# Kernel optimization log

Hardware: AMD Instinct MI355X
Metric: run time of the kernel (lower is better)

The kernel has to match this reference:

```python
import jax, jax.numpy as jnp
import numpy as np

B, T, C = 1, 2048, 2048
N_HEAD, N_KV = 32, 8
HD = C // N_HEAD            # 64
N_REP = N_HEAD // N_KV      # 4
WINDOW = 512                # sliding_window
N_GLOBAL = 16               # n_global_tokens


def setup_inputs() -> dict:
    key = jax.random.key(0)
    ks = jax.random.split(key, 5)
    x = jax.random.normal(ks[0], (B, T, C), jnp.float32)
    # standard RoPE frequency tables, shape (T, HD//2)
    inv_freq = 1.0 / (10000.0 ** (np.arange(0, HD, 2, dtype=np.float32) / HD))
    ang = np.outer(np.arange(T, dtype=np.float32), inv_freq)
    freqs_cos = jnp.asarray(np.cos(ang), jnp.float32)
    freqs_sin = jnp.asarray(np.sin(ang), jnp.float32)
    s = 0.02
    wq = jax.random.normal(ks[1], (C, C), jnp.float32) * s
    wk = jax.random.normal(ks[2], (N_KV * HD, C), jnp.float32) * s
    wv = jax.random.normal(ks[3], (N_KV * HD, C), jnp.float32) * s
    wo = jax.random.normal(ks[4], (C, C), jnp.float32) * s
    return {"x": x, "freqs_cos": freqs_cos, "freqs_sin": freqs_sin,
            "wq": wq, "wk": wk, "wv": wv, "wo": wo}


def _apply_rope(xh, fc, fs):
    # xh: (B, H, T, HD); fc/fs: (T, HD//2) broadcast over (B, H)
    xr = xh.reshape(*xh.shape[:-1], HD // 2, 2)
    x0, x1 = xr[..., 0], xr[..., 1]
    fc = fc[None, None]
    fs = fs[None, None]
    out = jnp.stack([x0 * fc - x1 * fs, x0 * fs + x1 * fc], axis=-1)
    return out.reshape(xh.shape)


def reference(x, freqs_cos, freqs_sin, wq, wk, wv, wo):
    Bx, Tx, Cx = x.shape
    q = (x @ wq.T).reshape(Bx, Tx, N_HEAD, HD).transpose(0, 2, 1, 3)   # (B,Hq,T,hd)
    k = (x @ wk.T).reshape(Bx, Tx, N_KV, HD).transpose(0, 2, 1, 3)     # (B,Hkv,T,hd)
    v = (x @ wv.T).reshape(Bx, Tx, N_KV, HD).transpose(0, 2, 1, 3)
    q = _apply_rope(q, freqs_cos, freqs_sin)
    k = _apply_rope(k, freqs_cos, freqs_sin)

    # GQA: group query heads over shared kv heads instead of repeat_kv
    qg = q.reshape(Bx, N_KV, N_REP, Tx, HD)
    scale = 1.0 / float(np.sqrt(HD))
    scores = jnp.einsum('bgrqd,bgkd->bgrqk', qg, k) * scale  # (B,G,R,T,T)

    # sliding-window causal mask with global tokens (kv_cache=None branch)
    q_pos = jnp.arange(Tx)[:, None]
    k_pos = jnp.arange(Tx)[None, :]
    mask = (k_pos <= q_pos) & (k_pos >= q_pos - (WINDOW - 1))
    mask = mask | (k_pos < N_GLOBAL)
    # note: global columns combined with causal rows always leave >=1 valid key
    scores = jnp.where(mask[None, None, None], scores, -jnp.inf)
    probs = jax.nn.softmax(scores, axis=-1)

    y = jnp.einsum('bgrqk,bgkd->bgrqd', probs, v)
    y = y.reshape(Bx, N_HEAD, Tx, HD).transpose(0, 2, 1, 3).reshape(Bx, Tx, Cx)
    return y @ wo.T  # dropout p=0 in eval
```

## Files before the change

### kernel.cpp

```cpp
#include <hip/hip_runtime.h>
#include <hip/hip_bf16.h>

using short8 = __attribute__((ext_vector_type(8))) short;
using f32x4  = __attribute__((ext_vector_type(4))) float;
using f32x16 = __attribute__((ext_vector_type(16))) float;
using int4v  = __attribute__((ext_vector_type(4))) int;

#define T_SEQ  2048
#define C_DIM  2048
#define NH     32
#define NKV    8
#define HD     64
#define WINDOW 512
#define NGLOB  16

__device__ inline ushort f2bf(float f) {
  union { float f; unsigned u; } v; v.f = f;
  unsigned u = v.u;
  u += 0x7fffu + ((u >> 16) & 1u);
  return (ushort)(u >> 16);
}
__device__ inline float bf2f(ushort h) {
  union { unsigned u; float f; } v; v.u = ((unsigned)h) << 16;
  return v.f;
}

__device__ __forceinline__ void gl_lds16(const ushort* g, ushort* l) {
  __builtin_amdgcn_global_load_lds(
      (const __attribute__((address_space(1))) void*)g,
      (__attribute__((address_space(3))) void*)l, 16, 0, 0);
}

__device__ __forceinline__ f32x16 zero16() {
  f32x16 v;
#pragma unroll
  for (int i = 0; i < 16; i++) v[i] = 0.f;
  return v;
}

__global__ void cvt_all(const float* __restrict__ s0, ushort* __restrict__ d0, int n0,
                        const float* __restrict__ s1, ushort* __restrict__ d1, int n1,
                        const float* __restrict__ s2, ushort* __restrict__ d2, int n2,
                        const float* __restrict__ s3, ushort* __restrict__ d3, int n3,
                        const float* __restrict__ s4, ushort* __restrict__ d4, int n4) {
  int total = n0 + n1 + n2 + n3 + n4;
  int stride = gridDim.x * blockDim.x;
  for (int i = blockIdx.x * blockDim.x + threadIdx.x; i < total; i += stride) {
    int j = i; const float* s; ushort* d;
    if (j < n0) { s = s0; d = d0; }
    else { j -= n0;
      if (j < n1) { s = s1; d = d1; }
      else { j -= n1;
        if (j < n2) { s = s2; d = d2; }
        else { j -= n2;
          if (j < n3) { s = s3; d = d3; }
          else { j -= n3; s = s4; d = d4; } } } }
    f32x4 a = *reinterpret_cast<const f32x4*>(s + (size_t)j * 8);
    f32x4 b = *reinterpret_cast<const f32x4*>(s + (size_t)j * 8 + 4);
    short8 o;
#pragma unroll
    for (int k = 0; k < 4; k++) { o[k] = (short)f2bf(a[k]); o[4 + k] = (short)f2bf(b[k]); }
    *reinterpret_cast<short8*>(d + (size_t)j * 8) = o;
  }
}

template <int MODE>
__global__ __launch_bounds__(512) void gemm2p(const ushort* __restrict__ A,
                                              const ushort* __restrict__ B0,
                                              const ushort* __restrict__ B1,
                                              const ushort* __restrict__ B2,
                                              void* __restrict__ C0,
                                              void* __restrict__ C1,
                                              void* __restrict__ C2,
                                              int K) {
  __shared__ ushort As[2][2][128][32];
  __shared__ ushort Bs[2][2][128][32];
  const int tid  = threadIdx.x;
  const int lane = tid & 63;
  const int wid  = tid >> 6;
  const int wr = wid >> 2, wc = wid & 3;
  const int r16 = lane & 15, g16 = (lane >> 4) & 3;
  const int bx = blockIdx.x, by = blockIdx.y;

  const ushort* Brow;
  void* Cout;
  int ldc, col0;
  if constexpr (MODE == 1) {
    if (bx < 16)      { Brow = B0 + (size_t)bx * 128 * K;        Cout = C0; ldc = 2048; col0 = bx * 128; }
    else if (bx < 20) { Brow = B1 + (size_t)(bx - 16) * 128 * K; Cout = C1; ldc = 512;  col0 = (bx - 16) * 128; }
    else              { Brow = B2 + (size_t)(bx - 20) * 128 * K; Cout = C2; ldc = 512;  col0 = (bx - 20) * 128; }
  } else {
    Brow = B0 + (size_t)bx * 128 * K; Cout = C0; ldc = 2048; col0 = bx * 128;
  }
  const ushort* Arow = A + (size_t)by * 128 * K;

  f32x4 acc[4][2];
#pragma unroll
  for (int i = 0; i < 4; i++)
#pragma unroll
    for (int j = 0; j < 2; j++) acc[i][j] = (f32x4){0.f, 0.f, 0.f, 0.f};

  const int srow = tid >> 2, scch = tid & 3;
  const int ssc  = scch ^ ((srow >> 1) & 3);
  const size_t agoff = (size_t)srow * K + ssc * 8;
  const int rchunk = (g16 ^ ((r16 >> 1) & 3)) * 8;

  const int nt = K >> 6;
  int d = 0;

#define STAGE(dd, k0)                                                         \
  {                                                                           \
    _Pragma("unroll") for (int kk = 0; kk < 2; kk++) {                        \
      gl_lds16(&Arow[agoff + (k0) + kk * 32], &As[dd][kk][srow][scch * 8]);   \
      gl_lds16(&Brow[agoff + (k0) + kk * 32], &Bs[dd][kk][srow][scch * 8]);   \
    }                                                                         \
  }

  STAGE(0, 0);
  __syncthreads();

  for (int t = 0; t < nt; ++t) {
    if (t + 1 < nt) STAGE(d ^ 1, (t + 1) * 64);
#pragma unroll
    for (int kk = 0; kk < 2; kk++) {
      short8 af[4], bfv[2];
#pragma unroll
      for (int i = 0; i < 4; i++)
        af[i] = *reinterpret_cast<const short8*>(&As[d][kk][wr * 64 + i * 16 + r16][rchunk]);
#pragma unroll
      for (int j = 0; j < 2; j++)
        bfv[j] = *reinterpret_cast<const short8*>(&Bs[d][kk][wc * 32 + j * 16 + r16][rchunk]);
#pragma unroll
      for (int i = 0; i < 4; i++)
#pragma unroll
        for (int j = 0; j < 2; j++)
          acc[i][j] = __builtin_amdgcn_mfma_f32_16x16x32_bf16(af[i], bfv[j], acc[i][j], 0, 0, 0);
    }
    __syncthreads();
    d ^= 1;
  }
#undef STAGE

#pragma unroll
  for (int i = 0; i < 4; i++)
#pragma unroll
    for (int j = 0; j < 2; j++) {
      int col = col0 + wc * 32 + j * 16 + r16;
#pragma unroll
      for (int r = 0; r < 4; r++) {
        int row = by * 128 + wr * 64 + i * 16 + g16 * 4 + r;
        if constexpr (MODE == 0) ((float*)Cout)[(size_t)row * ldc + col] = acc[i][j][r];
        else                     ((ushort*)Cout)[(size_t)row * ldc + col] = f2bf(acc[i][j][r]);
      }
    }
}

__global__ void rope2(ushort* __restrict__ Qb, ushort* __restrict__ Kb,
                      const float* __restrict__ fc, const float* __restrict__ fs) {
  int idx = blockIdx.x * blockDim.x + threadIdx.x;
  const int QN = T_SEQ * NH * 8;
  ushort* X; int t, hh, c, ld; float ksc;
  if (idx < QN) { X = Qb; c = idx & 7; hh = (idx >> 3) & 31; t = idx >> 8; ld = NH * HD;
                  ksc = 0.125f * 1.44269504089f; }
  else { idx -= QN; X = Kb; c = idx & 7; hh = (idx >> 3) & 7; t = idx >> 6; ld = NKV * HD;
         ksc = 1.0f; }
  size_t base = (size_t)t * ld + hh * HD + c * 8;
  short8 v = *reinterpret_cast<const short8*>(&X[base]);
  f32x4 cc = *reinterpret_cast<const f32x4*>(&fc[t * 32 + c * 4]);
  f32x4 ss = *reinterpret_cast<const f32x4*>(&fs[t * 32 + c * 4]);
  short8 o;
#pragma unroll
  for (int j = 0; j < 4; j++) {
    float x0 = bf2f((ushort)v[2 * j]), x1 = bf2f((ushort)v[2 * j + 1]);
    o[2 * j]     = (short)f2bf((x0 * cc[j] - x1 * ss[j]) * ksc);
    o[2 * j + 1] = (short)f2bf((x0 * ss[j] + x1 * cc[j]) * ksc);
  }
  *reinterpret_cast<short8*>(&X[base]) = o;
}

__global__ __launch_bounds__(256) void transpose_bf16(const ushort* __restrict__ in,
                                                      ushort* __restrict__ out,
                                                      int R, int Cc) {
  __shared__ ushort tile[64][72];
  int tr = blockIdx.y * 64, tc = blockIdx.x * 64;
  int tid = threadIdx.x;
#pragma unroll
  for (int s = 0; s < 2; s++) {
    int idx = tid + s * 256;
    int row = idx >> 3, c8 = idx & 7;
    short8 v = *reinterpret_cast<const short8*>(&in[(size_t)(tr + row) * Cc + tc + c8 * 8]);
#pragma unroll
    for (int j = 0; j < 8; j++) tile[row][c8 * 8 + j] = (ushort)v[j];
  }
  __syncthreads();
#pragma unroll
  for (int s = 0; s < 2; s++) {
    int idx = tid + s * 256;
    int orow = idx >> 3, c8 = idx & 7;
    short8 v;
#pragma unroll
    for (int j = 0; j < 8; j++) v[j] = (short)tile[c8 * 8 + j][orow];
    *reinterpret_cast<short8*>(&out[(size_t)(tc + orow) * R + tr + c8 * 8]) = v;
  }
}

__global__ __launch_bounds__(256) void attn32(const ushort* __restrict__ Q,
                                              const ushort* __restrict__ K,
                                              const ushort* __restrict__ Vt,
                                              ushort* __restrict__ Y) {
  __shared__ ushort Ot[4][32][72];
  const int lane = threadIdx.x & 63;
  const int wv   = threadIdx.x >> 6;
  const int g  = blockIdx.x >> 6;
  const int qt = blockIdx.x & 63;
  const int h  = g * 4 + wv;
  const int q0 = qt << 5;
  const int l31 = lane & 31, hi = lane >> 5;
  const int hi8 = hi << 3, hi4 = hi << 2;
  const int qrow = q0 + l31;

  short8 qf[4];
#pragma unroll
  for (int s = 0; s < 4; s++)
    qf[s] = *reinterpret_cast<const short8*>(&Q[(size_t)qrow * C_DIM + h * HD + s * 16 + hi8]);

  f32x16 o[2] = { zero16(), zero16() };
  float mrow = -1e30f, ssum = 0.f;

  auto pack8 = [&](const float* pp) -> short8 {
    unsigned wA, wB, wC, wD;
    asm("v_cvt_pk_bf16_f32 %0, %1, %2" : "=v"(wA) : "v"(pp[0]), "v"(pp[1]));
    asm("v_cvt_pk_bf16_f32 %0, %1, %2" : "=v"(wB) : "v"(pp[2]), "v"(pp[3]));
    asm("v_cvt_pk_bf16_f32 %0, %1, %2" : "=v"(wC) : "v"(pp[4]), "v"(pp[5]));
    asm("v_cvt_pk_bf16_f32 %0, %1, %2" : "=v"(wD) : "v"(pp[6]), "v"(pp[7]));
    asm("v_permlane32_swap_b32 %0, %1" : "+v"(wA), "+v"(wC));
    asm("v_permlane32_swap_b32 %0, %1" : "+v"(wB), "+v"(wD));
    int4v w4 = { (int)wA, (int)wB, (int)wC, (int)wD };
    return __builtin_bit_cast(short8, w4);
  };

#define LOADKV(kreg, vreg, kb)                                                     \
  {                                                                                \
    _Pragma("unroll") for (int s = 0; s < 4; s++)                                  \
      kreg[s] = *reinterpret_cast<const short8*>(                                  \
          &K[(size_t)((kb) + l31) * (NKV * HD) + g * HD + s * 16 + hi8]);          \
    _Pragma("unroll") for (int ntl = 0; ntl < 2; ntl++) {                          \
      const ushort* vp = &Vt[(size_t)(g * HD + ntl * 32 + l31) * T_SEQ + (kb) + hi8]; \
      vreg[2 * ntl]     = *reinterpret_cast<const short8*>(vp);                    \
      vreg[2 * ntl + 1] = *reinterpret_cast<const short8*>(vp + 16);               \
    }                                                                              \
  }

#define PROCESS(kreg, vreg, kb, domask)                                            \
  {                                                                                \
    f32x16 sa = zero16();                                                          \
    __builtin_amdgcn_s_setprio(1);                                                 \
    _Pragma("unroll") for (int s = 0; s < 4; s++)                                  \
      sa = __builtin_amdgcn_mfma_f32_32x32x16_bf16(kreg[s], qf[s], sa, 0, 0, 0);   \
    __builtin_amdgcn_s_setprio(0);                                                 \
    float p[16];                                                                   \
    _Pragma("unroll") for (int r = 0; r < 16; r++) p[r] = sa[r];                   \
    if (domask) {                                                                  \
      _Pragma("unroll") for (int r = 0; r < 16; r++) {                             \
        int kidx = (kb) + (r & 3) + 8 * (r >> 2) + hi4;                            \
        bool ok = ((kidx <= qrow) && (kidx >= qrow - (WINDOW - 1))) || (kidx < NGLOB); \
        p[r] = ok ? p[r] : -1e30f;                                                 \
      }                                                                            \
    }                                                                              \
    float t[16];                                                                   \
    _Pragma("unroll") for (int r = 0; r < 16; r++) t[r] = p[r];                    \
    _Pragma("unroll") for (int st = 1; st < 16; st <<= 1)                          \
      _Pragma("unroll") for (int i2 = 0; i2 < 16; i2 += 2 * st)                    \
        t[i2] = fmaxf(t[i2], t[i2 + st]);                                          \
    float pmax = fmaxf(t[0], __shfl_xor(t[0], 32));                                \
    if (!__all(pmax <= mrow + 8.0f)) {                                             \
      float mnew = fmaxf(mrow, pmax);                                              \
      float corr = exp2f(mrow - mnew);                                             \
      ssum *= corr;                                                                \
      _Pragma("unroll") for (int r = 0; r < 16; r++) { o[0][r] *= corr; o[1][r] *= corr; } \
      mrow = mnew;                                                                 \
    }                                                                              \
    _Pragma("unroll") for (int r = 0; r < 16; r++) p[r] = exp2f(p[r] - mrow);      \
    float su[16];                                                                  \
    _Pragma("unroll") for (int r = 0; r < 16; r++) su[r] = p[r];                   \
    _Pragma("unroll") for (int st = 1; st < 16; st <<= 1)                          \
      _Pragma("unroll") for (int i2 = 0; i2 < 16; i2 += 2 * st)                    \
        su[i2] += su[i2 + st];                                                     \
    ssum += su[0];                                                                 \
    short8 pb0 = pack8(&p[0]);                                                     \
    short8 pb1 = pack8(&p[8]);                                                     \
    __builtin_amdgcn_s_setprio(1);                                                 \
    o[0] = __builtin_amdgcn_mfma_f32_32x32x16_bf16(vreg[0], pb0, o[0], 0, 0, 0);   \
    o[0] = __builtin_amdgcn_mfma_f32_32x32x16_bf16(vreg[1], pb1, o[0], 0, 0, 0);   \
    o[1] = __builtin_amdgcn_mfma_f32_32x32x16_bf16(vreg[2], pb0, o[1], 0, 0, 0);   \
    o[1] = __builtin_amdgcn_mfma_f32_32x32x16_bf16(vreg[3], pb1, o[1], 0, 0, 0);   \
    __builtin_amdgcn_s_setprio(0);                                                 \
  }

  int wsr = (q0 - (WINDOW - 1)) >> 5;
  int wstart = (wsr < 1) ? 32 : (wsr << 5);
  int ntw = (q0 >= wstart) ? (((q0 - wstart) >> 5) + 1) : 0;
  const int NT = 1 + ntw;

  short8 kA[4], vA[4], kB[4], vB[4];
  LOADKV(kA, vA, 0);

  for (int i = 0; i < NT; i += 2) {
    int kb_i = (i == 0) ? 0 : wstart + (i - 1) * 32;
    if (i + 1 < NT) { int kb1 = wstart + i * 32; LOADKV(kB, vB, kb1); }
    bool m_i = (i == 0) || (kb_i < q0 - 480) || (kb_i == q0);
    PROCESS(kA, vA, kb_i, m_i);
    if (i + 1 < NT) {
      int kb1 = wstart + i * 32;
      if (i + 2 < NT) { int kb2 = wstart + (i + 1) * 32; LOADKV(kA, vA, kb2); }
      bool m1 = (kb1 < q0 - 480) || (kb1 == q0);
      PROCESS(kB, vB, kb1, m1);
    }
  }
#undef LOADKV
#undef PROCESS

  float stot = ssum + __shfl_xor(ssum, 32);
  float inv = 1.0f / stot;

#pragma unroll
  for (int ntl = 0; ntl < 2; ntl++)
#pragma unroll
    for (int r = 0; r < 16; r++) {
      int dim = ntl * 32 + (r & 3) + 8 * (r >> 2) + hi4;
      Ot[wv][l31][dim] = f2bf(o[ntl][r] * inv);
    }
  __syncthreads();
  int qq = lane >> 1, hf = lane & 1;
#pragma unroll
  for (int c = 0; c < 4; c++) {
    short8 vv = *reinterpret_cast<const short8*>(&Ot[wv][qq][hf * 32 + c * 8]);
    *reinterpret_cast<short8*>(&Y[(size_t)(q0 + qq) * C_DIM + h * HD + hf * 32 + c * 8]) = vv;
  }
}

extern "C" void kernel_launch(void* const* d_in, const int* in_sizes, int n_in,
                              void* d_out, int out_size, void* d_ws, size_t ws_size,
                              hipStream_t stream) {
  const float* x  = (const float*)d_in[0];
  const float* fc = (const float*)d_in[1];
  const float* fs = (const float*)d_in[2];
  const float* wq = (const float*)d_in[3];
  const float* wk = (const float*)d_in[4];
  const float* wv = (const float*)d_in[5];
  const float* wo = (const float*)d_in[6];
  float* out = (float*)d_out;

  const size_t SZ_X = (size_t)T_SEQ * C_DIM;
  const size_t SZ_W = (size_t)(NKV * HD) * C_DIM;

  ushort* xb  = (ushort*)d_ws;
  ushort* wqb = xb  + SZ_X;
  ushort* wkb = wqb + SZ_X;
  ushort* wvb = wkb + SZ_W;
  ushort* wob = wvb + SZ_W;
  ushort* Qb  = wob + SZ_X;
  ushort* Kb  = Qb  + SZ_X;
  ushort* Vb  = Kb  + SZ_W;
  ushort* Vt  = Vb  + SZ_W;
  ushort* Yb  = Vt  + SZ_W;

  cvt_all<<<1024, 256, 0, stream>>>(x,  xb,  (int)(SZ_X / 8),
                                    wq, wqb, (int)(SZ_X / 8),
                                    wk, wkb, (int)(SZ_W / 8),
                                    wv, wvb, (int)(SZ_W / 8),
                                    wo, wob, (int)(SZ_X / 8));

  gemm2p<1><<<dim3(24, 16), 512, 0, stream>>>(xb, wqb, wkb, wvb, Qb, Kb, Vb, C_DIM);

  rope2<<<(T_SEQ * (NH + NKV) * 8) / 256, 256, 0, stream>>>(Qb, Kb, fc, fs);
  transpose_bf16<<<dim3((NKV * HD) / 64, T_SEQ / 64), 256, 0, stream>>>(Vb, Vt, T_SEQ, NKV * HD);

  attn32<<<512, 256, 0, stream>>>(Qb, Kb, Vt, Yb);

  gemm2p<0><<<dim3(16, 16), 512, 0, stream>>>(Yb, wob, nullptr, nullptr, out, nullptr, nullptr, C_DIM);
}
```

Before: 135.2 us.

## Split attention KV range across two wave groups and fuse V transpose into GEMM

The V projection GEMM epilogue now writes V directly in transposed layout, which removes the separate transpose kernel and its extra global round trip. The attention kernel doubles its block to 512 threads: two waves per head each process half of the KV tiles, then merge their partial softmax state (max, sum, output) through shared memory before normalizing. This gives each query tile more parallelism and shortens the serial loop per wave. In exchange it adds shared-memory traffic, two block barriers and merge arithmetic, and the transposed epilogue issues narrow strided 8-byte stores.

```diff
diff --git a/kernel.cpp b/kernel.cpp
--- a/kernel.cpp
+++ b/kernel.cpp
@@ -1,6 +1,7 @@
 #include <hip/hip_runtime.h>
 #include <hip/hip_bf16.h>
 
+using short4v = __attribute__((ext_vector_type(4))) short;
 using short8 = __attribute__((ext_vector_type(8))) short;
 using f32x4  = __attribute__((ext_vector_type(4))) float;
 using f32x16 = __attribute__((ext_vector_type(16))) float;
@@ -85,10 +86,11 @@
   const ushort* Brow;
   void* Cout;
   int ldc, col0;
+  bool vtr = false;
   if constexpr (MODE == 1) {
     if (bx < 16)      { Brow = B0 + (size_t)bx * 128 * K;        Cout = C0; ldc = 2048; col0 = bx * 128; }
     else if (bx < 20) { Brow = B1 + (size_t)(bx - 16) * 128 * K; Cout = C1; ldc = 512;  col0 = (bx - 16) * 128; }
-    else              { Brow = B2 + (size_t)(bx - 20) * 128 * K; Cout = C2; ldc = 512;  col0 = (bx - 20) * 128; }
+    else              { Brow = B2 + (size_t)(bx - 20) * 128 * K; Cout = C2; ldc = 512;  col0 = (bx - 20) * 128; vtr = true; }
   } else {
     Brow = B0 + (size_t)bx * 128 * K; Cout = C0; ldc = 2048; col0 = bx * 128;
   }
@@ -146,11 +148,18 @@
 #pragma unroll
     for (int j = 0; j < 2; j++) {
       int col = col0 + wc * 32 + j * 16 + r16;
-#pragma unroll
-      for (int r = 0; r < 4; r++) {
-        int row = by * 128 + wr * 64 + i * 16 + g16 * 4 + r;
-        if constexpr (MODE == 0) ((float*)Cout)[(size_t)row * ldc + col] = acc[i][j][r];
-        else                     ((ushort*)Cout)[(size_t)row * ldc + col] = f2bf(acc[i][j][r]);
+      int row0 = by * 128 + wr * 64 + i * 16 + g16 * 4;
+      if (MODE == 1 && vtr) {
+        short4v tv;
+#pragma unroll
+        for (int r = 0; r < 4; r++) tv[r] = (short)f2bf(acc[i][j][r]);
+        *reinterpret_cast<short4v*>(&((ushort*)Cout)[(size_t)col * T_SEQ + row0]) = tv;
+      } else {
+#pragma unroll
+        for (int r = 0; r < 4; r++) {
+          if constexpr (MODE == 0) ((float*)Cout)[(size_t)(row0 + r) * ldc + col] = acc[i][j][r];
+          else                     ((ushort*)Cout)[(size_t)(row0 + r) * ldc + col] = f2bf(acc[i][j][r]);
+        }
       }
     }
 }
@@ -178,42 +187,21 @@
   *reinterpret_cast<short8*>(&X[base]) = o;
 }
 
-__global__ __launch_bounds__(256) void transpose_bf16(const ushort* __restrict__ in,
-                                                      ushort* __restrict__ out,
-                                                      int R, int Cc) {
-  __shared__ ushort tile[64][72];
-  int tr = blockIdx.y * 64, tc = blockIdx.x * 64;
-  int tid = threadIdx.x;
-#pragma unroll
-  for (int s = 0; s < 2; s++) {
-    int idx = tid + s * 256;
-    int row = idx >> 3, c8 = idx & 7;
-    short8 v = *reinterpret_cast<const short8*>(&in[(size_t)(tr + row) * Cc + tc + c8 * 8]);
-#pragma unroll
-    for (int j = 0; j < 8; j++) tile[row][c8 * 8 + j] = (ushort)v[j];
-  }
-  __syncthreads();
-#pragma unroll
-  for (int s = 0; s < 2; s++) {
-    int idx = tid + s * 256;
-    int orow = idx >> 3, c8 = idx & 7;
-    short8 v;
-#pragma unroll
-    for (int j = 0; j < 8; j++) v[j] = (short)tile[c8 * 8 + j][orow];
-    *reinterpret_cast<short8*>(&out[(size_t)(tc + orow) * R + tr + c8 * 8]) = v;
-  }
-}
-
-__global__ __launch_bounds__(256) void attn32(const ushort* __restrict__ Q,
-                                              const ushort* __restrict__ K,
-                                              const ushort* __restrict__ Vt,
-                                              ushort* __restrict__ Y) {
+__global__ __launch_bounds__(512, 4) void attn32(const ushort* __restrict__ Q,
+                                                 const ushort* __restrict__ K,
+                                                 const ushort* __restrict__ Vt,
+                                                 ushort* __restrict__ Y) {
+  __shared__ float oS[4][64][33];
+  __shared__ float mS[4][32];
+  __shared__ float sS[4][64];
   __shared__ ushort Ot[4][32][72];
   const int lane = threadIdx.x & 63;
   const int wv   = threadIdx.x >> 6;
+  const int hh   = wv & 3;
+  const int split = wv >> 2;
   const int g  = blockIdx.x >> 6;
   const int qt = blockIdx.x & 63;
-  const int h  = g * 4 + wv;
+  const int h  = g * 4 + hh;
   const int q0 = qt << 5;
   const int l31 = lane & 31, hi = lane >> 5;
   const int hi8 = hi << 3, hi4 = hi << 2;
@@ -301,41 +289,71 @@
   int wstart = (wsr < 1) ? 32 : (wsr << 5);
   int ntw = (q0 >= wstart) ? (((q0 - wstart) >> 5) + 1) : 0;
   const int NT = 1 + ntw;
+  const int ihalf = (NT + 1) >> 1;
+  const int i0 = split ? ihalf : 0;
+  const int i1 = split ? NT : ihalf;
+
+#define KBOF(i) ((i) == 0 ? 0 : wstart + ((i) - 1) * 32)
+#define MSK(i)  ((i) == 0 || (KBOF(i) < q0 - 480) || (KBOF(i) == q0))
 
   short8 kA[4], vA[4], kB[4], vB[4];
-  LOADKV(kA, vA, 0);
-
-  for (int i = 0; i < NT; i += 2) {
-    int kb_i = (i == 0) ? 0 : wstart + (i - 1) * 32;
-    if (i + 1 < NT) { int kb1 = wstart + i * 32; LOADKV(kB, vB, kb1); }
-    bool m_i = (i == 0) || (kb_i < q0 - 480) || (kb_i == q0);
-    PROCESS(kA, vA, kb_i, m_i);
-    if (i + 1 < NT) {
-      int kb1 = wstart + i * 32;
-      if (i + 2 < NT) { int kb2 = wstart + (i + 1) * 32; LOADKV(kA, vA, kb2); }
-      bool m1 = (kb1 < q0 - 480) || (kb1 == q0);
-      PROCESS(kB, vB, kb1, m1);
+  if (i0 < i1) {
+    LOADKV(kA, vA, KBOF(i0));
+    for (int i = i0; i < i1; i += 2) {
+      if (i + 1 < i1) LOADKV(kB, vB, KBOF(i + 1));
+      PROCESS(kA, vA, KBOF(i), MSK(i));
+      if (i + 1 < i1) {
+        if (i + 2 < i1) LOADKV(kA, vA, KBOF(i + 2));
+        PROCESS(kB, vB, KBOF(i + 1), MSK(i + 1));
+      }
     }
   }
 #undef LOADKV
 #undef PROCESS
-
-  float stot = ssum + __shfl_xor(ssum, 32);
-  float inv = 1.0f / stot;
-
-#pragma unroll
-  for (int ntl = 0; ntl < 2; ntl++)
-#pragma unroll
-    for (int r = 0; r < 16; r++) {
-      int dim = ntl * 32 + (r & 3) + 8 * (r >> 2) + hi4;
-      Ot[wv][l31][dim] = f2bf(o[ntl][r] * inv);
+#undef KBOF
+#undef MSK
+
+  if (split == 1) {
+    if (hi == 0) mS[hh][l31] = mrow;
+    sS[hh][lane] = ssum;
+#pragma unroll
+    for (int ntl = 0; ntl < 2; ntl++)
+#pragma unroll
+      for (int r = 0; r < 16; r++) oS[hh][lane][ntl * 16 + r] = o[ntl][r];
+  }
+  __syncthreads();
+
+  if (split == 0) {
+    float mB = mS[hh][l31];
+    float sB = sS[hh][lane];
+    float mN = fmaxf(mrow, mB);
+    float cA = exp2f(mrow - mN), cB = exp2f(mB - mN);
+    ssum = ssum * cA + sB * cB;
+#pragma unroll
+    for (int ntl = 0; ntl < 2; ntl++)
+#pragma unroll
+      for (int r = 0; r < 16; r++)
+        o[ntl][r] = o[ntl][r] * cA + oS[hh][lane][ntl * 16 + r] * cB;
+
+    float stot = ssum + __shfl_xor(ssum, 32);
+    float inv = 1.0f / stot;
+#pragma unroll
+    for (int ntl = 0; ntl < 2; ntl++)
+#pragma unroll
+      for (int r = 0; r < 16; r++) {
+        int dim = ntl * 32 + (r & 3) + 8 * (r >> 2) + hi4;
+        Ot[hh][l31][dim] = f2bf(o[ntl][r] * inv);
+      }
+  }
+  __syncthreads();
+
+  if (split == 0) {
+    int qq = lane >> 1, hf = lane & 1;
+#pragma unroll
+    for (int c = 0; c < 4; c++) {
+      short8 vv = *reinterpret_cast<const short8*>(&Ot[hh][qq][hf * 32 + c * 8]);
+      *reinterpret_cast<short8*>(&Y[(size_t)(q0 + qq) * C_DIM + h * HD + hf * 32 + c * 8]) = vv;
     }
-  __syncthreads();
-  int qq = lane >> 1, hf = lane & 1;
-#pragma unroll
-  for (int c = 0; c < 4; c++) {
-    short8 vv = *reinterpret_cast<const short8*>(&Ot[wv][qq][hf * 32 + c * 8]);
-    *reinterpret_cast<short8*>(&Y[(size_t)(q0 + qq) * C_DIM + h * HD + hf * 32 + c * 8]) = vv;
   }
 }
 
@@ -361,8 +379,7 @@
   ushort* wob = wvb + SZ_W;
   ushort* Qb  = wob + SZ_X;
   ushort* Kb  = Qb  + SZ_X;
-  ushort* Vb  = Kb  + SZ_W;
-  ushort* Vt  = Vb  + SZ_W;
+  ushort* Vt  = Kb  + SZ_W;
   ushort* Yb  = Vt  + SZ_W;
 
   cvt_all<<<1024, 256, 0, stream>>>(x,  xb,  (int)(SZ_X / 8),
@@ -371,12 +388,11 @@
                                     wv, wvb, (int)(SZ_W / 8),
                                     wo, wob, (int)(SZ_X / 8));
 
-  gemm2p<1><<<dim3(24, 16), 512, 0, stream>>>(xb, wqb, wkb, wvb, Qb, Kb, Vb, C_DIM);
+  gemm2p<1><<<dim3(24, 16), 512, 0, stream>>>(xb, wqb, wkb, wvb, Qb, Kb, Vt, C_DIM);
 
   rope2<<<(T_SEQ * (NH + NKV) * 8) / 256, 256, 0, stream>>>(Qb, Kb, fc, fs);
-  transpose_bf16<<<dim3((NKV * HD) / 64, T_SEQ / 64), 256, 0, stream>>>(Vb, Vt, T_SEQ, NKV * HD);
-
-  attn32<<<512, 256, 0, stream>>>(Qb, Kb, Vt, Yb);
+
+  attn32<<<512, 512, 0, stream>>>(Qb, Kb, Vt, Yb);
 
   gemm2p<0><<<dim3(16, 16), 512, 0, stream>>>(Yb, wob, nullptr, nullptr, out, nullptr, nullptr, C_DIM);
 }
```

After: 158.2 us. +17.1%, slower.
